# Kernel tuning notes

Hardware: AMD Instinct MI355X
Metric: run time of the kernel (lower is better)

Reference implementation:

```python
import jax, jax.numpy as jnp
import numpy as np

NUM_NODES = 50000
D_IN, D_HID, D_OUT = 128, 128, 40
NUM_EDGES = 800000


def setup_inputs() -> dict:
    key = jax.random.key(0)
    ks = jax.random.split(key, 10)
    x = jax.random.normal(ks[0], (NUM_NODES, D_IN), dtype=jnp.float32)
    edge_index = jax.random.randint(ks[1], (2, NUM_EDGES), 0, NUM_NODES, dtype=jnp.int64)
    # GCNConv weights (lin: in -> out), glorot-style init; bias init zeros per bias_init
    def glorot(k, fan_in, fan_out):
        lim = np.sqrt(6.0 / (fan_in + fan_out)).astype(np.float32)
        return jax.random.uniform(k, (fan_in, fan_out), jnp.float32, -lim, lim)
    W0 = glorot(ks[2], D_IN, D_HID)
    b0 = jnp.zeros((D_HID,), jnp.float32)
    W1 = glorot(ks[3], D_HID, D_HID)
    b1 = jnp.zeros((D_HID,), jnp.float32)
    W2 = glorot(ks[4], D_HID, D_OUT)
    b2 = jnp.zeros((D_OUT,), jnp.float32)
    return {"x": x, "edge_index": edge_index,
            "W0": W0, "b0": b0, "W1": W1, "b1": b1, "W2": W2, "b2": b2}


def _gcn_conv(h, src, dst, W, b):
    # linear projection then gather from source nodes, scatter-add to dest nodes
    hW = h @ W                                   # [N, out]
    msg = jnp.take(hW, src, axis=0)              # [E, out]
    agg = jax.ops.segment_sum(msg, dst, num_segments=NUM_NODES)  # [N, out]
    return agg + b


def reference(x, edge_index, W0, b0, W1, b1, W2, b2):
    src, dst = edge_index[0], edge_index[1]
    h = jax.nn.relu(_gcn_conv(x, src, dst, W0, b0))
    h = jax.nn.relu(_gcn_conv(h, src, dst, W1, b1))
    return _gcn_conv(h, src, dst, W2, b2)
```

## Files before the change

### kernel.cpp

```cpp
#include <hip/hip_runtime.h>

#define NN 50000
#define EE 800000

#define BKT 196
#define GB  334
#define EPB 2396
#define CAP 5120

typedef unsigned short u16;
typedef unsigned int u32;
typedef __attribute__((ext_vector_type(8))) short short8;
typedef __attribute__((ext_vector_type(4))) float f32x4;
typedef __attribute__((ext_vector_type(4))) unsigned short ushort4v;

__device__ __forceinline__ float b2f(u16 u) {
    return __uint_as_float(((unsigned)u) << 16);
}
__device__ __forceinline__ u16 f2b(float f) {
    unsigned u = __float_as_uint(f);
    return (u16)((u + 0x7FFF + ((u >> 16) & 1)) >> 16);
}

__global__ __launch_bounds__(256) void hist_prep(
    const int* __restrict__ dst, int* __restrict__ BBC,
    const float* __restrict__ W0, const float* __restrict__ W1,
    const float* __restrict__ W2, u16* __restrict__ Wf, int E)
{
    __shared__ int cnt[BKT];
    const int g = blockIdx.x, t = threadIdx.x;
    if (g < GB) {
        for (int b = t; b < BKT; b += 256) cnt[b] = 0;
        __syncthreads();
        const int beg = g * EPB, end = min(E, beg + EPB);
        for (int e = beg + t; e < end; e += 256)
            atomicAdd(&cnt[dst[e] >> 8], 1);
        __syncthreads();
        for (int b = t; b < BKT; b += 256) BBC[b * GB + g] = cnt[b];
    } else {
        int u = (g - GB) * 4 + (t >> 6);
        int set = u >> 5, nt2 = (u >> 2) & 7, kt = u & 3;
        int lane = t & 63;
        const float* W = (set == 0) ? W0 : (set == 1) ? W1 : W2;
        int ld = (set == 2) ? 40 : 128;
        int ncols = (set == 2) ? 40 : 128;
        int n = nt2 * 16 + (lane & 15);
        int kb = kt * 32 + (lane >> 4) * 8;
        u16* dw = Wf + set * 16384 + (size_t)((nt2 * 4 + kt) * 64 + lane) * 8;
#pragma unroll
        for (int j = 0; j < 8; j++) {
            float v = (n < ncols) ? W[(kb + j) * ld + n] : 0.f;
            dw[j] = f2b(v);
        }
    }
}

__global__ __launch_bounds__(1024) void block_scan(
    const int* __restrict__ in, int* __restrict__ out,
    int* __restrict__ blockSums, int M)
{
    __shared__ int sh[1024];
    const int t = threadIdx.x;
    const int idx = blockIdx.x * 1024 + t;
    const int v = (idx < M) ? in[idx] : 0;
    sh[t] = v;
    __syncthreads();
    for (int d = 1; d < 1024; d <<= 1) {
        int u = (t >= d) ? sh[t - d] : 0;
        __syncthreads();
        sh[t] += u;
        __syncthreads();
    }
    if (idx < M) out[idx] = sh[t] - v;
    if (t == 1023) blockSums[blockIdx.x] = sh[t];
}

__global__ __launch_bounds__(1024) void add_base_scan(
    int* __restrict__ S, const int* __restrict__ blockSums, int M, int nb)
{
    __shared__ int sb[64];
    const int t = threadIdx.x;
    if (t < 64) sb[t] = (t < nb) ? blockSums[t] : 0;
    __syncthreads();
    if (t == 0) {
        int run = 0;
        for (int i = 0; i < 64; i++) { int v = sb[i]; sb[i] = run; run += v; }
    }
    __syncthreads();
    const int base = sb[blockIdx.x];
    const int idx = blockIdx.x * 1024 + t;
    if (idx < M) S[idx] += base;
}

__global__ __launch_bounds__(256) void scatter_gemm0(
    const int* __restrict__ src, const int* __restrict__ dst,
    const int* __restrict__ S, u32* __restrict__ pairs,
    const float* __restrict__ A, const u16* __restrict__ Wf,
    u16* __restrict__ out, int N, int E)
{
    __shared__ int cur[BKT];
    const int t = threadIdx.x;
    if (blockIdx.x < GB) {
        const int g = blockIdx.x;
        for (int b = t; b < BKT; b += 256) cur[b] = S[b * GB + g];
        __syncthreads();
        const int beg = g * EPB, end = min(E, beg + EPB);
        for (int e = beg + t; e < end; e += 256) {
            int d = dst[e];
            int pos = atomicAdd(&cur[d >> 8], 1);
            pairs[pos] = ((u32)src[e] << 8) | (u32)(d & 255);
        }
        return;
    }
    const int bx = blockIdx.x - GB;
    const int wave = t >> 6;
    const int lane = t & 63;
    const int m = lane & 15;
    const int q = lane >> 4;
    const int rowBase = bx * 64 + wave * 16;
    const int arow = rowBase + m;
    const bool rowOk = (arow < N);

    short8 af[4];
#pragma unroll
    for (int kt = 0; kt < 4; kt++) {
        if (rowOk) {
            float4 lo = *(const float4*)(A + (size_t)arow * 128 + kt * 32 + q * 8);
            float4 hi = *(const float4*)(A + (size_t)arow * 128 + kt * 32 + q * 8 + 4);
            short8 v;
            v[0] = (short)f2b(lo.x); v[1] = (short)f2b(lo.y);
            v[2] = (short)f2b(lo.z); v[3] = (short)f2b(lo.w);
            v[4] = (short)f2b(hi.x); v[5] = (short)f2b(hi.y);
            v[6] = (short)f2b(hi.z); v[7] = (short)f2b(hi.w);
            af[kt] = v;
        } else {
            af[kt] = (short8)0;
        }
    }

    f32x4 acc[8];
#pragma unroll
    for (int nt = 0; nt < 8; nt++) acc[nt] = (f32x4)0.f;

#pragma unroll
    for (int kt = 0; kt < 4; kt++) {
#pragma unroll
        for (int nt = 0; nt < 8; nt++) {
            short8 bf = *(const short8*)(Wf + (size_t)((nt * 4 + kt) * 64 + lane) * 8);
            acc[nt] = __builtin_amdgcn_mfma_f32_16x16x32_bf16(af[kt], bf, acc[nt], 0, 0, 0);
        }
    }

#pragma unroll
    for (int nt = 0; nt < 8; nt++) {
#pragma unroll
        for (int r = 0; r < 4; r++) {
            int orow = rowBase + q * 4 + r;
            if (orow < N) out[(size_t)orow * 128 + nt * 16 + m] = f2b(acc[nt][r]);
        }
    }
}

__global__ __launch_bounds__(256) void bucket_sort(
    const u32* __restrict__ pairs, const int* __restrict__ S,
    int* __restrict__ off, int* __restrict__ csr, int N, int E)
{
    __shared__ int sdeg[256];
    __shared__ int sex[256];
    __shared__ int scur[256];
    __shared__ int stage[CAP];
    const int b = blockIdx.x, t = threadIdx.x;
    const int base = S[b * GB];
    const int end  = (b == BKT - 1) ? E : S[(b + 1) * GB];
    const int cnt = end - base;

    sdeg[t] = 0;
    __syncthreads();
    for (int i = t; i < cnt; i += 256)
        atomicAdd(&sdeg[pairs[base + i] & 255], 1);
    __syncthreads();

    int v = sdeg[t];
    sex[t] = v;
    __syncthreads();
    for (int d = 1; d < 256; d <<= 1) {
        int u = (t >= d) ? sex[t - d] : 0;
        __syncthreads();
        sex[t] += u;
        __syncthreads();
    }
    const int excl = sex[t] - v;
    const int node = b * 256 + t;
    if (node < N) off[node] = base + excl;
    if (b == BKT - 1 && t == 0) off[N] = E;
    scur[t] = excl;
    __syncthreads();

    if (cnt <= CAP) {
        for (int i = t; i < cnt; i += 256) {
            u32 p = pairs[base + i];
            int pos = atomicAdd(&scur[p & 255], 1);
            stage[pos] = (int)(p >> 8);
        }
        __syncthreads();
        for (int i = t; i < cnt; i += 256) csr[base + i] = stage[i];
    } else {
        for (int i = t; i < cnt; i += 256) {
            u32 p = pairs[base + i];
            int pos = atomicAdd(&scur[p & 255], 1);
            csr[base + pos] = (int)(p >> 8);
        }
    }
}

template<int NT, int OSTRIDE>
__global__ __launch_bounds__(512) void agg_gemm_t(
    const u16* __restrict__ val, const int* __restrict__ off,
    const int* __restrict__ csr, const float* __restrict__ bias,
    const u16* __restrict__ Wf, u16* __restrict__ out, int N)
{
    __shared__ u16 A[64][136];
    const int tid = threadIdx.x;
    const int rowBase = blockIdx.x * 64;

    {
        const int c = tid & 15;
        const int nl = tid >> 4;
        float4 bA = *(const float4*)(bias + c * 8);
        float4 bB = *(const float4*)(bias + c * 8 + 4);
        float bb[8] = {bA.x, bA.y, bA.z, bA.w, bB.x, bB.y, bB.z, bB.w};
#pragma unroll
        for (int g = 0; g < 2; g++) {
            const int lrow = g * 32 + nl;
            const int node = rowBase + lrow;
            float a0[8] = {0, 0, 0, 0, 0, 0, 0, 0};
            float a1[8] = {0, 0, 0, 0, 0, 0, 0, 0};
            if (node < N) {
                const int beg = off[node], end = off[node + 1];
                int i = beg;
                for (; i + 3 < end; i += 4) {
                    int s0 = csr[i];
                    int s1 = csr[i + 1];
                    int s2 = csr[i + 2];
                    int s3 = csr[i + 3];
                    short8 v0 = *(const short8*)(val + (size_t)s0 * 128 + c * 8);
                    short8 v1 = *(const short8*)(val + (size_t)s1 * 128 + c * 8);
                    short8 v2 = *(const short8*)(val + (size_t)s2 * 128 + c * 8);
                    short8 v3 = *(const short8*)(val + (size_t)s3 * 128 + c * 8);
#pragma unroll
                    for (int j = 0; j < 8; j++) {
                        a0[j] += b2f((u16)v0[j]) + b2f((u16)v2[j]);
                        a1[j] += b2f((u16)v1[j]) + b2f((u16)v3[j]);
                    }
                }
                for (; i < end; i++) {
                    int s0 = csr[i];
                    short8 v0 = *(const short8*)(val + (size_t)s0 * 128 + c * 8);
#pragma unroll
                    for (int j = 0; j < 8; j++) a0[j] += b2f((u16)v0[j]);
                }
            }
            short8 o;
#pragma unroll
            for (int j = 0; j < 8; j++)
                o[j] = (short)f2b(fmaxf(a0[j] + a1[j] + bb[j], 0.f));
            *(short8*)&A[lrow][c * 8] = o;
        }
    }
    __syncthreads();

    const int wave = tid >> 6;
    const int lane = tid & 63;
    const int m = lane & 15;
    const int q = lane >> 4;
    const int rg = wave & 3;
    const int ch = wave >> 2;
    const int lrow = rg * 16 + m;

    short8 af[4];
#pragma unroll
    for (int kt = 0; kt < 4; kt++)
        af[kt] = *(const short8*)&A[lrow][kt * 32 + q * 8];

    constexpr int NTH = (NT + 1) / 2;
    const int ntB = ch ? NTH : 0;
    const int ntE = ch ? NT : NTH;

    f32x4 acc[NTH];
#pragma unroll
    for (int i = 0; i < NTH; i++) acc[i] = (f32x4)0.f;

#pragma unroll
    for (int kt = 0; kt < 4; kt++) {
        for (int nt = ntB; nt < ntE; nt++) {
            short8 bf = *(const short8*)(Wf + (size_t)((nt * 4 + kt) * 64 + lane) * 8);
            acc[nt - ntB] = __builtin_amdgcn_mfma_f32_16x16x32_bf16(af[kt], bf, acc[nt - ntB], 0, 0, 0);
        }
    }

    for (int nt = ntB; nt < ntE; nt++) {
#pragma unroll
        for (int r = 0; r < 4; r++) {
            int orow = rowBase + rg * 16 + q * 4 + r;
            if (orow < N) out[(size_t)orow * OSTRIDE + nt * 16 + m] = f2b(acc[nt - ntB][r]);
        }
    }
}

__global__ __launch_bounds__(256) void agg40b(
    const u16* __restrict__ val, const int* __restrict__ off,
    const int* __restrict__ csr, const float* __restrict__ b2,
    float* __restrict__ out, int N)
{
    const int c = threadIdx.x & 15;
    const int node = blockIdx.x * 16 + (threadIdx.x >> 4);
    if (node >= N || c >= 10) return;
    const int beg = off[node], end = off[node + 1];

    float a0[4] = {0, 0, 0, 0};
    float a1[4] = {0, 0, 0, 0};
    int i = beg;
    for (; i + 1 < end; i += 2) {
        int s0 = csr[i];
        int s1 = csr[i + 1];
        ushort4v v0 = *(const ushort4v*)(val + (size_t)s0 * 48 + c * 4);
        ushort4v v1 = *(const ushort4v*)(val + (size_t)s1 * 48 + c * 4);
        a0[0] += b2f(v0.x); a0[1] += b2f(v0.y); a0[2] += b2f(v0.z); a0[3] += b2f(v0.w);
        a1[0] += b2f(v1.x); a1[1] += b2f(v1.y); a1[2] += b2f(v1.z); a1[3] += b2f(v1.w);
    }
    if (i < end) {
        int s0 = csr[i];
        ushort4v v0 = *(const ushort4v*)(val + (size_t)s0 * 48 + c * 4);
        a0[0] += b2f(v0.x); a0[1] += b2f(v0.y); a0[2] += b2f(v0.z); a0[3] += b2f(v0.w);
    }
    float4 b = *(const float4*)(b2 + c * 4);
    float4 r;
    r.x = a0[0] + a1[0] + b.x;
    r.y = a0[1] + a1[1] + b.y;
    r.z = a0[2] + a1[2] + b.z;
    r.w = a0[3] + a1[3] + b.w;
    *(float4*)(out + (size_t)node * 40 + c * 4) = r;
}

extern "C" void kernel_launch(void* const* d_in, const int* in_sizes, int n_in,
                              void* d_out, int out_size, void* d_ws, size_t ws_size,
                              hipStream_t stream)
{
    const float* x  = (const float*)d_in[0];
    const int*   ei = (const int*)d_in[1];
    const float* W0 = (const float*)d_in[2];
    const float* b0 = (const float*)d_in[3];
    const float* W1 = (const float*)d_in[4];
    const float* b1 = (const float*)d_in[5];
    const float* W2 = (const float*)d_in[6];
    const float* b2 = (const float*)d_in[7];
    float* out = (float*)d_out;

    const int N = NN, E = EE;
    const int* src = ei;
    const int* dst = ei + E;

    char* ws = (char*)d_ws;
    u16* t       = (u16*)ws;
    u16* tB      = (u16*)(ws + 12800000);
    u16* t2      = (u16*)(ws + 25600000);
    u16* Wf      = (u16*)(ws + 30400000);
    int* off     = (int*)(ws + 30500000);
    int* csr     = (int*)(ws + 30700008);
    int* BBC     = (int*)(ws + 33900008);
    int* S       = (int*)(ws + 34161864);
    int* blkSums = (int*)(ws + 34423720);
    u32* pairs   = (u32*)(ws + 34423976);

    const int M = BKT * GB;
    const int nScan = (M + 1023) / 1024;
    const int tileGrid = (N + 63) / 64;
    const int agg40Grid = (N + 15) / 16;

    hist_prep<<<GB + 24, 256, 0, stream>>>(dst, BBC, W0, W1, W2, Wf, E);
    block_scan<<<nScan, 1024, 0, stream>>>(BBC, S, blkSums, M);
    add_base_scan<<<nScan, 1024, 0, stream>>>(S, blkSums, M, nScan);
    scatter_gemm0<<<GB + tileGrid, 256, 0, stream>>>(src, dst, S, pairs,
                                                     x, Wf, t, N, E);
    bucket_sort<<<BKT, 256, 0, stream>>>(pairs, S, off, csr, N, E);

    agg_gemm_t<8, 128><<<tileGrid, 512, 0, stream>>>(t, off, csr, b0,
                                                     Wf + 16384, tB, N);
    agg_gemm_t<3, 48><<<tileGrid, 512, 0, stream>>>(tB, off, csr, b1,
                                                    Wf + 32768, t2, N);
    agg40b<<<agg40Grid, 256, 0, stream>>>(t2, off, csr, b2, out, N);
}
```

Baseline: 209.7 us.

## Replace global histogram scan with atomic bucket cursors and shrink layer-2 row stride

Removes the separate histogram kernel and the two-kernel global prefix scan. Each scatter block now counts its bucket occupancy locally and reserves space with one global atomicAdd per bucket into fixed-capacity bucket slots (CAPB). bucket_sort derives bucket bases with an in-block scan over the 196 bucket counts. This cuts three launches and the extra pass over dst, at the cost of nondeterministic pair order within a bucket and overflow risk if a bucket exceeds 6144 edges. Separately, the 40-column intermediate is stored with stride 40 instead of 48, which reduces gather bytes in the last aggregation.

```diff
diff --git a/kernel.cpp b/kernel.cpp
--- a/kernel.cpp
+++ b/kernel.cpp
@@ -6,6 +6,7 @@
 #define BKT 196
 #define GB  334
 #define EPB 2396
+#define CAPB 6144
 #define CAP 5120
 
 typedef unsigned short u16;
@@ -22,89 +23,52 @@
     return (u16)((u + 0x7FFF + ((u >> 16) & 1)) >> 16);
 }
 
-__global__ __launch_bounds__(256) void hist_prep(
-    const int* __restrict__ dst, int* __restrict__ BBC,
+__global__ __launch_bounds__(256) void prep_init(
     const float* __restrict__ W0, const float* __restrict__ W1,
-    const float* __restrict__ W2, u16* __restrict__ Wf, int E)
-{
-    __shared__ int cnt[BKT];
+    const float* __restrict__ W2, u16* __restrict__ Wf,
+    int* __restrict__ gCur)
+{
     const int g = blockIdx.x, t = threadIdx.x;
-    if (g < GB) {
-        for (int b = t; b < BKT; b += 256) cnt[b] = 0;
-        __syncthreads();
-        const int beg = g * EPB, end = min(E, beg + EPB);
-        for (int e = beg + t; e < end; e += 256)
-            atomicAdd(&cnt[dst[e] >> 8], 1);
-        __syncthreads();
-        for (int b = t; b < BKT; b += 256) BBC[b * GB + g] = cnt[b];
-    } else {
-        int u = (g - GB) * 4 + (t >> 6);
-        int set = u >> 5, nt2 = (u >> 2) & 7, kt = u & 3;
-        int lane = t & 63;
-        const float* W = (set == 0) ? W0 : (set == 1) ? W1 : W2;
-        int ld = (set == 2) ? 40 : 128;
-        int ncols = (set == 2) ? 40 : 128;
-        int n = nt2 * 16 + (lane & 15);
-        int kb = kt * 32 + (lane >> 4) * 8;
-        u16* dw = Wf + set * 16384 + (size_t)((nt2 * 4 + kt) * 64 + lane) * 8;
-#pragma unroll
-        for (int j = 0; j < 8; j++) {
-            float v = (n < ncols) ? W[(kb + j) * ld + n] : 0.f;
-            dw[j] = f2b(v);
-        }
-    }
-}
-
-__global__ __launch_bounds__(1024) void block_scan(
-    const int* __restrict__ in, int* __restrict__ out,
-    int* __restrict__ blockSums, int M)
-{
-    __shared__ int sh[1024];
-    const int t = threadIdx.x;
-    const int idx = blockIdx.x * 1024 + t;
-    const int v = (idx < M) ? in[idx] : 0;
-    sh[t] = v;
-    __syncthreads();
-    for (int d = 1; d < 1024; d <<= 1) {
-        int u = (t >= d) ? sh[t - d] : 0;
-        __syncthreads();
-        sh[t] += u;
-        __syncthreads();
-    }
-    if (idx < M) out[idx] = sh[t] - v;
-    if (t == 1023) blockSums[blockIdx.x] = sh[t];
-}
-
-__global__ __launch_bounds__(1024) void add_base_scan(
-    int* __restrict__ S, const int* __restrict__ blockSums, int M, int nb)
-{
-    __shared__ int sb[64];
-    const int t = threadIdx.x;
-    if (t < 64) sb[t] = (t < nb) ? blockSums[t] : 0;
-    __syncthreads();
-    if (t == 0) {
-        int run = 0;
-        for (int i = 0; i < 64; i++) { int v = sb[i]; sb[i] = run; run += v; }
-    }
-    __syncthreads();
-    const int base = sb[blockIdx.x];
-    const int idx = blockIdx.x * 1024 + t;
-    if (idx < M) S[idx] += base;
+    if (g == 24) {
+        if (t < BKT) gCur[t] = t * CAPB;
+        return;
+    }
+    int u = g * 4 + (t >> 6);
+    int set = u >> 5, nt2 = (u >> 2) & 7, kt = u & 3;
+    int lane = t & 63;
+    const float* W = (set == 0) ? W0 : (set == 1) ? W1 : W2;
+    int ld = (set == 2) ? 40 : 128;
+    int ncols = (set == 2) ? 40 : 128;
+    int n = nt2 * 16 + (lane & 15);
+    int kb = kt * 32 + (lane >> 4) * 8;
+    u16* dw = Wf + set * 16384 + (size_t)((nt2 * 4 + kt) * 64 + lane) * 8;
+#pragma unroll
+    for (int j = 0; j < 8; j++) {
+        float v = (n < ncols) ? W[(kb + j) * ld + n] : 0.f;
+        dw[j] = f2b(v);
+    }
 }
 
 __global__ __launch_bounds__(256) void scatter_gemm0(
     const int* __restrict__ src, const int* __restrict__ dst,
-    const int* __restrict__ S, u32* __restrict__ pairs,
+    int* __restrict__ gCur, u32* __restrict__ pairs,
     const float* __restrict__ A, const u16* __restrict__ Wf,
     u16* __restrict__ out, int N, int E)
 {
+    __shared__ int cnt[BKT];
     __shared__ int cur[BKT];
     const int t = threadIdx.x;
     if (blockIdx.x < GB) {
         const int g = blockIdx.x;
-        for (int b = t; b < BKT; b += 256) cur[b] = S[b * GB + g];
+        for (int b = t; b < BKT; b += 256) cnt[b] = 0;
         __syncthreads();
         const int beg = g * EPB, end = min(E, beg + EPB);
+        for (int e = beg + t; e < end; e += 256)
+            atomicAdd(&cnt[dst[e] >> 8], 1);
+        __syncthreads();
+        for (int b = t; b < BKT; b += 256)
+            cur[b] = atomicAdd(&gCur[b], cnt[b]);
+        __syncthreads();
         for (int e = beg + t; e < end; e += 256) {
             int d = dst[e];
             int pos = atomicAdd(&cur[d >> 8], 1);
@@ -162,7 +126,7 @@
 }
 
 __global__ __launch_bounds__(256) void bucket_sort(
-    const u32* __restrict__ pairs, const int* __restrict__ S,
+    const u32* __restrict__ pairs, const int* __restrict__ gCur,
     int* __restrict__ off, int* __restrict__ csr, int N, int E)
 {
     __shared__ int sdeg[256];
@@ -170,14 +134,28 @@
     __shared__ int scur[256];
     __shared__ int stage[CAP];
     const int b = blockIdx.x, t = threadIdx.x;
-    const int base = S[b * GB];
-    const int end  = (b == BKT - 1) ? E : S[(b + 1) * GB];
-    const int cnt = end - base;
+
+    int c0 = (t < BKT) ? (gCur[t] - t * CAPB) : 0;
+    sex[t] = c0;
+    __syncthreads();
+    for (int d = 1; d < 256; d <<= 1) {
+        int u = (t >= d) ? sex[t - d] : 0;
+        __syncthreads();
+        sex[t] += u;
+        __syncthreads();
+    }
+    __shared__ int sBase, sCnt;
+    if (t == b) { sBase = sex[t] - c0; sCnt = c0; }
+    __syncthreads();
+    const int base = sBase;
+    const int cnt = sCnt;
+    const int pbase = b * CAPB;
+    __syncthreads();
 
     sdeg[t] = 0;
     __syncthreads();
     for (int i = t; i < cnt; i += 256)
-        atomicAdd(&sdeg[pairs[base + i] & 255], 1);
+        atomicAdd(&sdeg[pairs[pbase + i] & 255], 1);
     __syncthreads();
 
     int v = sdeg[t];
@@ -198,7 +176,7 @@
 
     if (cnt <= CAP) {
         for (int i = t; i < cnt; i += 256) {
-            u32 p = pairs[base + i];
+            u32 p = pairs[pbase + i];
             int pos = atomicAdd(&scur[p & 255], 1);
             stage[pos] = (int)(p >> 8);
         }
@@ -206,14 +184,14 @@
         for (int i = t; i < cnt; i += 256) csr[base + i] = stage[i];
     } else {
         for (int i = t; i < cnt; i += 256) {
-            u32 p = pairs[base + i];
+            u32 p = pairs[pbase + i];
             int pos = atomicAdd(&scur[p & 255], 1);
             csr[base + pos] = (int)(p >> 8);
         }
     }
 }
 
-template<int NT, int OSTRIDE>
+template<int NT, int OSTRIDE, int OCOLS>
 __global__ __launch_bounds__(512) void agg_gemm_t(
     const u16* __restrict__ val, const int* __restrict__ off,
     const int* __restrict__ csr, const float* __restrict__ bias,
@@ -299,10 +277,13 @@
     }
 
     for (int nt = ntB; nt < ntE; nt++) {
-#pragma unroll
-        for (int r = 0; r < 4; r++) {
-            int orow = rowBase + rg * 16 + q * 4 + r;
-            if (orow < N) out[(size_t)orow * OSTRIDE + nt * 16 + m] = f2b(acc[nt - ntB][r]);
+        const int col = nt * 16 + m;
+        if (col < OCOLS) {
+#pragma unroll
+            for (int r = 0; r < 4; r++) {
+                int orow = rowBase + rg * 16 + q * 4 + r;
+                if (orow < N) out[(size_t)orow * OSTRIDE + col] = f2b(acc[nt - ntB][r]);
+            }
         }
     }
 }
@@ -323,14 +304,14 @@
     for (; i + 1 < end; i += 2) {
         int s0 = csr[i];
         int s1 = csr[i + 1];
-        ushort4v v0 = *(const ushort4v*)(val + (size_t)s0 * 48 + c * 4);
-        ushort4v v1 = *(const ushort4v*)(val + (size_t)s1 * 48 + c * 4);
+        ushort4v v0 = *(const ushort4v*)(val + (size_t)s0 * 40 + c * 4);
+        ushort4v v1 = *(const ushort4v*)(val + (size_t)s1 * 40 + c * 4);
         a0[0] += b2f(v0.x); a0[1] += b2f(v0.y); a0[2] += b2f(v0.z); a0[3] += b2f(v0.w);
         a1[0] += b2f(v1.x); a1[1] += b2f(v1.y); a1[2] += b2f(v1.z); a1[3] += b2f(v1.w);
     }
     if (i < end) {
         int s0 = csr[i];
-        ushort4v v0 = *(const ushort4v*)(val + (size_t)s0 * 48 + c * 4);
+        ushort4v v0 = *(const ushort4v*)(val + (size_t)s0 * 40 + c * 4);
         a0[0] += b2f(v0.x); a0[1] += b2f(v0.y); a0[2] += b2f(v0.z); a0[3] += b2f(v0.w);
     }
     float4 b = *(const float4*)(b2 + c * 4);
@@ -361,32 +342,26 @@
     const int* dst = ei + E;
 
     char* ws = (char*)d_ws;
-    u16* t       = (u16*)ws;
-    u16* tB      = (u16*)(ws + 12800000);
-    u16* t2      = (u16*)(ws + 25600000);
-    u16* Wf      = (u16*)(ws + 30400000);
-    int* off     = (int*)(ws + 30500000);
-    int* csr     = (int*)(ws + 30700008);
-    int* BBC     = (int*)(ws + 33900008);
-    int* S       = (int*)(ws + 34161864);
-    int* blkSums = (int*)(ws + 34423720);
-    u32* pairs   = (u32*)(ws + 34423976);
-
-    const int M = BKT * GB;
-    const int nScan = (M + 1023) / 1024;
+    u16* t     = (u16*)ws;
+    u16* tB    = (u16*)(ws + 12800000);
+    u16* t2    = (u16*)(ws + 25600000);
+    u16* Wf    = (u16*)(ws + 29600000);
+    int* off   = (int*)(ws + 29700000);
+    int* csr   = (int*)(ws + 29900008);
+    int* gCur  = (int*)(ws + 33100008);
+    u32* pairs = (u32*)(ws + 33100800);
+
     const int tileGrid = (N + 63) / 64;
     const int agg40Grid = (N + 15) / 16;
 
-    hist_prep<<<GB + 24, 256, 0, stream>>>(dst, BBC, W0, W1, W2, Wf, E);
-    block_scan<<<nScan, 1024, 0, stream>>>(BBC, S, blkSums, M);
-    add_base_scan<<<nScan, 1024, 0, stream>>>(S, blkSums, M, nScan);
-    scatter_gemm0<<<GB + tileGrid, 256, 0, stream>>>(src, dst, S, pairs,
+    prep_init<<<25, 256, 0, stream>>>(W0, W1, W2, Wf, gCur);
+    scatter_gemm0<<<GB + tileGrid, 256, 0, stream>>>(src, dst, gCur, pairs,
                                                      x, Wf, t, N, E);
-    bucket_sort<<<BKT, 256, 0, stream>>>(pairs, S, off, csr, N, E);
-
-    agg_gemm_t<8, 128><<<tileGrid, 512, 0, stream>>>(t, off, csr, b0,
-                                                     Wf + 16384, tB, N);
-    agg_gemm_t<3, 48><<<tileGrid, 512, 0, stream>>>(tB, off, csr, b1,
-                                                    Wf + 32768, t2, N);
+    bucket_sort<<<BKT, 256, 0, stream>>>(pairs, gCur, off, csr, N, E);
+
+    agg_gemm_t<8, 128, 128><<<tileGrid, 512, 0, stream>>>(t, off, csr, b0,
+                                                          Wf + 16384, tB, N);
+    agg_gemm_t<3, 40, 40><<<tileGrid, 512, 0, stream>>>(tB, off, csr, b1,
+                                                        Wf + 32768, t2, N);
     agg40b<<<agg40Grid, 256, 0, stream>>>(t2, off, csr, b2, out, N);
 }
```

Result: no change. 207.7 us, median of 2 (-1.0%).
